# Kernel tuning notes

Hardware: AMD Instinct MI355X
Metric: run time of the kernel (lower is better)

## Reference

```python
import jax, jax.numpy as jnp
import numpy as np

NUM_HEADS = 4
KERNEL = 7


def setup_inputs() -> dict:
    key = jax.random.key(0)
    k = jax.random.split(key, 6)
    B, H, W, C = 4, 64, 64, 128
    kk = KERNEL
    x = jax.random.normal(k[0], (B, H, W, C), dtype=jnp.float32)
    w_qkv = jax.random.normal(k[1], (C, 3 * C), dtype=jnp.float32) * 0.02
    b_qkv = jnp.zeros((3 * C,), dtype=jnp.float32)
    rpb = jax.random.normal(k[2], (NUM_HEADS, 2 * kk - 1, 2 * kk - 1), dtype=jnp.float32) * 0.02
    w_proj = jax.random.normal(k[3], (C, C), dtype=jnp.float32) * 0.02
    b_proj = jnp.zeros((C,), dtype=jnp.float32)
    return {"x": x, "w_qkv": w_qkv, "b_qkv": b_qkv, "rpb": rpb,
            "w_proj": w_proj, "b_proj": b_proj}


def reference(x, w_qkv, b_qkv, rpb, w_proj, b_proj):
    B, H, W, C = x.shape
    nh, k = NUM_HEADS, KERNEL
    d = C // nh
    scale = d ** -0.5

    qkv = x @ w_qkv + b_qkv                      # [B,H,W,3C]
    q, kt, v = jnp.split(qkv, 3, axis=-1)
    q = q.reshape(B, H, W, nh, d) * scale
    kt = kt.reshape(B, H, W, nh, d)
    v = v.reshape(B, H, W, nh, d)

    # NATTEN window: centered, clamped at borders (window never shrinks)
    start_h = jnp.clip(jnp.arange(H) - k // 2, 0, H - k)
    start_w = jnp.clip(jnp.arange(W) - k // 2, 0, W - k)
    idx_h = start_h[:, None] + jnp.arange(k)     # [H,k] key rows per query row
    idx_w = start_w[:, None] + jnp.arange(k)     # [W,k]

    kn = kt[:, idx_h][:, :, :, idx_w]            # [B,H,k,W,k,nh,d]
    vn = v[:, idx_h][:, :, :, idx_w]             # [B,H,k,W,k,nh,d]

    scores = jnp.einsum('bxyhd,bxiyjhd->bxyhij', q, kn)  # [B,H,W,nh,k,k]

    # relative position bias: index = (key_pos - query_pos) + (k-1)
    bh = idx_h - jnp.arange(H)[:, None] + (k - 1)        # [H,k] in [0,2k-2]
    bw = idx_w - jnp.arange(W)[:, None] + (k - 1)        # [W,k]
    bias = rpb[:, bh[:, None, :, None], bw[None, :, None, :]]  # [nh,H,W,k,k]
    scores = scores + jnp.transpose(bias, (1, 2, 0, 3, 4))

    attn = jax.nn.softmax(scores.reshape(B, H, W, nh, k * k), axis=-1)
    attn = attn.reshape(B, H, W, nh, k, k)

    out = jnp.einsum('bxyhij,bxiyjhd->bxyhd', attn, vn)  # [B,H,W,nh,d]
    out = out.reshape(B, H, W, C) @ w_proj + b_proj
    return out
```

## Files before the change

### kernel.cpp

```cpp
#include <hip/hip_runtime.h>
#include <cstddef>
#include <cstdint>

#define Hdim 64
#define Wdim 64
#define NH 4
#define DH 32
#define KW 7
#define QSCALE 0.17677669529663687f

typedef _Float16 v2h __attribute__((ext_vector_type(2)));
typedef _Float16 half8 __attribute__((ext_vector_type(8)));
typedef float f32x4 __attribute__((ext_vector_type(4)));

#if defined(__has_builtin)
#if __has_builtin(__builtin_amdgcn_fdot2)
#define HAVE_FDOT2 1
#endif
#endif

__device__ __forceinline__ float fdot2acc(v2h a, v2h b, float c) {
#ifdef HAVE_FDOT2
    return __builtin_amdgcn_fdot2(a, b, c, false);
#else
    return fmaf((float)a.x, (float)b.x, fmaf((float)a.y, (float)b.y, c));
#endif
}

union F16x8 {
    uint4 u;
    v2h h[4];
};

__global__ __launch_bounds__(256) void prep_weights(
    const float* __restrict__ wq, const float* __restrict__ wp,
    _Float16* __restrict__ wqT, _Float16* __restrict__ wpT)
{
    __shared__ float Ts[64][65];
    int blk = blockIdx.x;
    const float* src;
    _Float16* dst;
    int N, kt, nt;
    if (blk < 12) { src = wq; dst = wqT; N = 384; kt = blk / 6; nt = blk % 6; }
    else { blk -= 12; src = wp; dst = wpT; N = 128; kt = blk >> 1; nt = blk & 1; }
    const int k0 = kt * 64, n0 = nt * 64;
    const int tid = threadIdx.x;

#pragma unroll
    for (int it = 0; it < 16; ++it) {
        int idx = it * 256 + tid;
        int r = idx >> 6, c = idx & 63;
        Ts[r][c] = src[(size_t)(k0 + r) * N + n0 + c];
    }
    __syncthreads();
#pragma unroll
    for (int it = 0; it < 2; ++it) {
        int idx = it * 256 + tid;
        int n = idx >> 3;
        int kq = (idx & 7) * 8;
        _Float16 tmp[8];
#pragma unroll
        for (int j = 0; j < 8; ++j) tmp[j] = (_Float16)Ts[kq + j][n];
        *(uint4*)(dst + (size_t)(n0 + n) * 128 + k0 + kq) = *(const uint4*)tmp;
    }
}

__global__ __launch_bounds__(256) void gemm_qkv_mfma(
    const float* __restrict__ A,
    const _Float16* __restrict__ WT,
    const float* __restrict__ bias,
    _Float16* __restrict__ qkvh)
{
    __shared__ _Float16 As[64 * 136];
    const int m0 = blockIdx.x * 64;
    const int sel = blockIdx.y;
    const int n0 = sel * 128;
    const int tid = threadIdx.x;
    const int wv = tid >> 6;
    const int ln = tid & 15;
    const int quad = (tid & 63) >> 4;

#pragma unroll
    for (int it = 0; it < 8; ++it) {
        int idx = it * 256 + tid;
        int m = idx >> 5;
        int kq = (idx & 31) * 4;
        float4 a = *(const float4*)(A + (size_t)(m0 + m) * 128 + kq);
        _Float16 t[4] = {(_Float16)a.x, (_Float16)a.y, (_Float16)a.z, (_Float16)a.w};
        *(uint2*)(As + m * 136 + kq) = *(const uint2*)t;
    }
    __syncthreads();

    f32x4 acc[8] = {};
    const int mrow = wv * 16 + ln;
#pragma unroll
    for (int ks = 0; ks < 4; ++ks) {
        const half8 af = *(const half8*)(As + mrow * 136 + ks * 32 + quad * 8);
#pragma unroll
        for (int nt = 0; nt < 8; ++nt) {
            const half8 bf = *(const half8*)(WT + (size_t)(n0 + nt * 16 + ln) * 128 + ks * 32 + quad * 8);
            acc[nt] = __builtin_amdgcn_mfma_f32_16x16x32_f16(af, bf, acc[nt], 0, 0, 0);
        }
    }
    __syncthreads();

    const float qscale = (sel == 0) ? QSCALE : 1.0f;
#pragma unroll
    for (int nt = 0; nt < 8; ++nt) {
        const int n = nt * 16 + ln;
        const float bv = bias[n0 + n];
#pragma unroll
        for (int r = 0; r < 4; ++r) {
            const int m = wv * 16 + quad * 4 + r;
            As[m * 136 + n] = (_Float16)((acc[nt][r] + bv) * qscale);
        }
    }
    __syncthreads();

    const int b = m0 >> 12;
    const int yx0 = m0 & 4095;
#pragma unroll
    for (int h = 0; h < 4; ++h) {
        const int r = tid >> 2;
        const int c = tid & 3;
        uint4 v = *(const uint4*)(As + r * 136 + h * 32 + c * 8);
        *(uint4*)(qkvh + (((size_t)sel * 16 + b * 4 + h) * 4096 + yx0 + r) * 32 + c * 8) = v;
    }
}

#define ATS 8
#define AMAXPOS 196
#define KST 40

__global__ __launch_bounds__(256, 4) void local_attn(
    const _Float16* __restrict__ qkvh,
    const float* __restrict__ rpb,
    float* __restrict__ outp)
{
    __shared__ _Float16 kS[AMAXPOS * KST];
    __shared__ _Float16 vS[AMAXPOS * KST];
    __shared__ float rS[169];

    const int bh = blockIdx.x;
    const int h = bh & 3;
    const int ty0 = blockIdx.y * ATS;
    const int tx0 = blockIdx.z * ATS;
    const int tid = threadIdx.x;

    const int lo_h = max(0, min(ty0 - 3, Hdim - KW));
    const int hi_h = min(ty0 + ATS - 4, Hdim - KW) + KW - 1;
    const int lo_w = max(0, min(tx0 - 3, Wdim - KW));
    const int hi_w = min(tx0 + ATS - 4, Wdim - KW) + KW - 1;
    const int ch = hi_h - lo_h + 1;
    const int cw = hi_w - lo_w + 1;
    const int npos = ch * cw;

    const _Float16* kbase = qkvh + (size_t)(16 + bh) * 131072;
    const _Float16* vbase = qkvh + (size_t)(32 + bh) * 131072;

    for (int idx = tid; idx < npos * 4; idx += 256) {
        const int pos = idx >> 2;
        const int c = idx & 3;
        const int ry = pos / cw;
        const int rx = pos - ry * cw;
        const size_t g = ((size_t)(lo_h + ry) * Wdim + (lo_w + rx)) * 32 + c * 8;
        *(uint4*)(kS + pos * KST + c * 8) = *(const uint4*)(kbase + g);
        *(uint4*)(vS + pos * KST + c * 8) = *(const uint4*)(vbase + g);
    }
    for (int i = tid; i < 169; i += 256) rS[i] = rpb[h * 169 + i];
    __syncthreads();

    const int p = tid >> 2;
    const int q = tid & 3;
    const int py = p >> 3, px = p & 7;
    const int y = ty0 + py, x = tx0 + px;
    const int sh = max(0, min(y - 3, Hdim - KW));
    const int sw = max(0, min(x - 3, Wdim - KW));
    const int rb = sh - lo_h;
    const int cb = sw - lo_w;
    const int bh0 = sh - y + 6;
    const int bw0 = sw - x + 6;

    F16x8 qf;
    qf.u = *(const uint4*)(qkvh + (size_t)bh * 131072 + ((size_t)y * Wdim + x) * 32 + q * 8);

    float sc[49];
#pragma unroll
    for (int i = 0; i < KW; ++i) {
        const _Float16* kp = kS + ((rb + i) * cw + cb) * KST + q * 8;
        const int bi = (bh0 + i) * 13 + bw0;
#pragma unroll
        for (int j = 0; j < KW; ++j) {
            F16x8 kf;
            kf.u = *(const uint4*)(kp + j * KST);
            float s = fdot2acc(qf.h[0], kf.h[0],
                      fdot2acc(qf.h[1], kf.h[1],
                      fdot2acc(qf.h[2], kf.h[2],
                      fdot2acc(qf.h[3], kf.h[3], 0.0f))));
            s += __shfl_xor(s, 1);
            s += __shfl_xor(s, 2);
            sc[i * KW + j] = s + rS[bi + j];
        }
    }

    float mx = sc[0];
#pragma unroll
    for (int t = 1; t < 49; ++t) mx = fmaxf(mx, sc[t]);
    float l = 0.f;
#pragma unroll
    for (int t = 0; t < 49; ++t) { sc[t] = __expf(sc[t] - mx); l += sc[t]; }
    const float inv = 1.f / l;

    float o[8] = {};
#pragma unroll
    for (int i = 0; i < KW; ++i) {
        const _Float16* vp = vS + ((rb + i) * cw + cb) * KST + q * 8;
#pragma unroll
        for (int j = 0; j < KW; ++j) {
            F16x8 vf;
            vf.u = *(const uint4*)(vp + j * KST);
            const float w = sc[i * KW + j] * inv;
#pragma unroll
            for (int d = 0; d < 4; ++d) {
                o[2 * d + 0] = fmaf(w, (float)vf.h[d].x, o[2 * d + 0]);
                o[2 * d + 1] = fmaf(w, (float)vf.h[d].y, o[2 * d + 1]);
            }
        }
    }

    const size_t pix = (size_t)(bh >> 2) * 4096 + (size_t)y * Wdim + x;
    float* dst = outp + pix * 128 + h * DH + q * 8;
    *(float4*)(dst)     = make_float4(o[0], o[1], o[2], o[3]);
    *(float4*)(dst + 4) = make_float4(o[4], o[5], o[6], o[7]);
}

__global__ __launch_bounds__(256) void gemm_proj_mfma(
    const float* __restrict__ Af,
    const _Float16* __restrict__ WT,
    const float* __restrict__ bias,
    float* __restrict__ C)
{
    __shared__ float Cs[64 * 132];
    _Float16* As = (_Float16*)Cs;

    const int m0 = blockIdx.x * 64;
    const int tid = threadIdx.x;
    const int wv = tid >> 6;
    const int ln = tid & 15;
    const int quad = (tid & 63) >> 4;

#pragma unroll
    for (int it = 0; it < 8; ++it) {
        int idx = it * 256 + tid;
        int m = idx >> 5;
        int kq = (idx & 31) * 4;
        float4 a = *(const float4*)(Af + (size_t)(m0 + m) * 128 + kq);
        _Float16 t[4] = {(_Float16)a.x, (_Float16)a.y, (_Float16)a.z, (_Float16)a.w};
        *(uint2*)(As + m * 136 + kq) = *(const uint2*)t;
    }
    __syncthreads();

    f32x4 acc[8] = {};
    const int mrow = wv * 16 + ln;
#pragma unroll
    for (int ks = 0; ks < 4; ++ks) {
        const half8 af = *(const half8*)(As + mrow * 136 + ks * 32 + quad * 8);
#pragma unroll
        for (int nt = 0; nt < 8; ++nt) {
            const half8 bf = *(const half8*)(WT + (size_t)(nt * 16 + ln) * 128 + ks * 32 + quad * 8);
            acc[nt] = __builtin_amdgcn_mfma_f32_16x16x32_f16(af, bf, acc[nt], 0, 0, 0);
        }
    }
    __syncthreads();

#pragma unroll
    for (int nt = 0; nt < 8; ++nt) {
        const int n = nt * 16 + ln;
        const float bv = bias[n];
#pragma unroll
        for (int r = 0; r < 4; ++r) {
            const int m = wv * 16 + quad * 4 + r;
            Cs[m * 132 + n] = acc[nt][r] + bv;
        }
    }
    __syncthreads();

#pragma unroll
    for (int it = 0; it < 8; ++it) {
        int idx = it * 256 + tid;
        int m = idx >> 5;
        int c = idx & 31;
        float4 v = *(const float4*)(Cs + m * 132 + c * 4);
        *(float4*)(C + (size_t)(m0 + m) * 128 + c * 4) = v;
    }
}

extern "C" void kernel_launch(void* const* d_in, const int* in_sizes, int n_in,
                              void* d_out, int out_size, void* d_ws, size_t ws_size,
                              hipStream_t stream) {
    const float* x      = (const float*)d_in[0];
    const float* w_qkv  = (const float*)d_in[1];
    const float* b_qkv  = (const float*)d_in[2];
    const float* rpb    = (const float*)d_in[3];
    const float* w_proj = (const float*)d_in[4];
    const float* b_proj = (const float*)d_in[5];
    float* out = (float*)d_out;

    char* ws = (char*)d_ws;
    _Float16* qkvh = (_Float16*)ws;
    float* attnf   = (float*)(ws + 12582912);
    _Float16* wqT  = (_Float16*)(ws + 12582912 + 8388608);
    _Float16* wpT  = (_Float16*)(ws + 12582912 + 8388608 + 98304);

    dim3 blk(256);
    prep_weights<<<16, blk, 0, stream>>>(w_qkv, w_proj, wqT, wpT);
    gemm_qkv_mfma<<<dim3(16384 / 64, 3), blk, 0, stream>>>(x, wqT, b_qkv, qkvh);
    local_attn<<<dim3(16, Hdim / ATS, Wdim / ATS), blk, 0, stream>>>(qkvh, rpb, attnf);
    gemm_proj_mfma<<<dim3(16384 / 64, 1), blk, 0, stream>>>(attnf, wpT, b_proj, out);
}
```

Baseline: 119.7 us.

## Fuse neighborhood attention with output projection in one 1024-thread block

Merges the local attention kernel and the projection GEMM into a single kernel. Each block now handles all four heads for an 8x8 pixel tile, so the attention result stays in shared memory as fp16 and feeds MFMA projection tiles directly. This removes the fp32 intermediate buffer write/read and one kernel launch. In exchange the block uses about 107KB of shared memory and 1024 threads, which limits occupancy to roughly one block per CU, and the grid shrinks to 256 blocks.

```diff
diff --git a/kernel.cpp b/kernel.cpp
--- a/kernel.cpp
+++ b/kernel.cpp
@@ -130,19 +130,23 @@
 
 #define ATS 8
 #define AMAXPOS 196
-#define KST 40
-
-__global__ __launch_bounds__(256, 4) void local_attn(
+#define PSTR 136
+
+__global__ __launch_bounds__(1024) void attn_proj(
     const _Float16* __restrict__ qkvh,
     const float* __restrict__ rpb,
+    const _Float16* __restrict__ wpT,
+    const float* __restrict__ bproj,
     float* __restrict__ outp)
 {
-    __shared__ _Float16 kS[AMAXPOS * KST];
-    __shared__ _Float16 vS[AMAXPOS * KST];
-    __shared__ float rS[169];
-
-    const int bh = blockIdx.x;
-    const int h = bh & 3;
+    __shared__ __align__(16) char arena[AMAXPOS * PSTR * 2 * 2 + 169 * NH * 4];
+    _Float16* kS = (_Float16*)arena;
+    _Float16* vS = kS + AMAXPOS * PSTR;
+    float* rS = (float*)(arena + AMAXPOS * PSTR * 2 * 2);
+    _Float16* Of = kS;
+    float* Cs = (float*)vS;
+
+    const int b = blockIdx.x;
     const int ty0 = blockIdx.y * ATS;
     const int tx0 = blockIdx.z * ATS;
     const int tid = threadIdx.x;
@@ -155,22 +159,24 @@
     const int cw = hi_w - lo_w + 1;
     const int npos = ch * cw;
 
-    const _Float16* kbase = qkvh + (size_t)(16 + bh) * 131072;
-    const _Float16* vbase = qkvh + (size_t)(32 + bh) * 131072;
-
-    for (int idx = tid; idx < npos * 4; idx += 256) {
-        const int pos = idx >> 2;
-        const int c = idx & 3;
+    for (int idx = tid; idx < npos * 16; idx += 1024) {
+        const int pos = idx >> 4;
+        const int sub = idx & 15;
+        const int hh = sub >> 2;
+        const int cc = sub & 3;
         const int ry = pos / cw;
         const int rx = pos - ry * cw;
-        const size_t g = ((size_t)(lo_h + ry) * Wdim + (lo_w + rx)) * 32 + c * 8;
-        *(uint4*)(kS + pos * KST + c * 8) = *(const uint4*)(kbase + g);
-        *(uint4*)(vS + pos * KST + c * 8) = *(const uint4*)(vbase + g);
-    }
-    for (int i = tid; i < 169; i += 256) rS[i] = rpb[h * 169 + i];
-    __syncthreads();
-
-    const int p = tid >> 2;
+        const size_t g = ((size_t)(lo_h + ry) * Wdim + (lo_w + rx)) * 32 + cc * 8;
+        const size_t kpl = ((size_t)(16 + b * 4 + hh)) * 131072;
+        const size_t vpl = ((size_t)(32 + b * 4 + hh)) * 131072;
+        *(uint4*)(kS + pos * PSTR + hh * 32 + cc * 8) = *(const uint4*)(qkvh + kpl + g);
+        *(uint4*)(vS + pos * PSTR + hh * 32 + cc * 8) = *(const uint4*)(qkvh + vpl + g);
+    }
+    for (int i = tid; i < 169 * NH; i += 1024) rS[i] = rpb[i];
+    __syncthreads();
+
+    const int h = tid >> 8;
+    const int p = (tid >> 2) & 63;
     const int q = tid & 3;
     const int py = p >> 3, px = p & 7;
     const int y = ty0 + py, x = tx0 + px;
@@ -180,19 +186,21 @@
     const int cb = sw - lo_w;
     const int bh0 = sh - y + 6;
     const int bw0 = sw - x + 6;
+    const int hq = h * 32 + q * 8;
 
     F16x8 qf;
-    qf.u = *(const uint4*)(qkvh + (size_t)bh * 131072 + ((size_t)y * Wdim + x) * 32 + q * 8);
+    qf.u = *(const uint4*)(qkvh + ((size_t)(b * 4 + h)) * 131072 +
+                           ((size_t)y * Wdim + x) * 32 + q * 8);
 
     float sc[49];
 #pragma unroll
     for (int i = 0; i < KW; ++i) {
-        const _Float16* kp = kS + ((rb + i) * cw + cb) * KST + q * 8;
-        const int bi = (bh0 + i) * 13 + bw0;
+        const _Float16* kp = kS + ((rb + i) * cw + cb) * PSTR + hq;
+        const int bi = h * 169 + (bh0 + i) * 13 + bw0;
 #pragma unroll
         for (int j = 0; j < KW; ++j) {
             F16x8 kf;
-            kf.u = *(const uint4*)(kp + j * KST);
+            kf.u = *(const uint4*)(kp + j * PSTR);
             float s = fdot2acc(qf.h[0], kf.h[0],
                       fdot2acc(qf.h[1], kf.h[1],
                       fdot2acc(qf.h[2], kf.h[2],
@@ -214,11 +222,11 @@
     float o[8] = {};
 #pragma unroll
     for (int i = 0; i < KW; ++i) {
-        const _Float16* vp = vS + ((rb + i) * cw + cb) * KST + q * 8;
+        const _Float16* vp = vS + ((rb + i) * cw + cb) * PSTR + hq;
 #pragma unroll
         for (int j = 0; j < KW; ++j) {
             F16x8 vf;
-            vf.u = *(const uint4*)(vp + j * KST);
+            vf.u = *(const uint4*)(vp + j * PSTR);
             const float w = sc[i * KW + j] * inv;
 #pragma unroll
             for (int d = 0; d < 4; ++d) {
@@ -228,70 +236,55 @@
         }
     }
 
-    const size_t pix = (size_t)(bh >> 2) * 4096 + (size_t)y * Wdim + x;
-    float* dst = outp + pix * 128 + h * DH + q * 8;
-    *(float4*)(dst)     = make_float4(o[0], o[1], o[2], o[3]);
-    *(float4*)(dst + 4) = make_float4(o[4], o[5], o[6], o[7]);
-}
-
-__global__ __launch_bounds__(256) void gemm_proj_mfma(
-    const float* __restrict__ Af,
-    const _Float16* __restrict__ WT,
-    const float* __restrict__ bias,
-    float* __restrict__ C)
-{
-    __shared__ float Cs[64 * 132];
-    _Float16* As = (_Float16*)Cs;
-
-    const int m0 = blockIdx.x * 64;
-    const int tid = threadIdx.x;
-    const int wv = tid >> 6;
+    __syncthreads();
+    {
+        _Float16 oh[8];
+#pragma unroll
+        for (int d = 0; d < 8; ++d) oh[d] = (_Float16)o[d];
+        *(uint4*)(Of + p * PSTR + hq) = *(const uint4*)oh;
+    }
+    __syncthreads();
+
+    const int wvid = tid >> 6;
+    const int mt = wvid >> 2;
+    const int nh2 = wvid & 3;
     const int ln = tid & 15;
     const int quad = (tid & 63) >> 4;
 
-#pragma unroll
-    for (int it = 0; it < 8; ++it) {
-        int idx = it * 256 + tid;
-        int m = idx >> 5;
-        int kq = (idx & 31) * 4;
-        float4 a = *(const float4*)(Af + (size_t)(m0 + m) * 128 + kq);
-        _Float16 t[4] = {(_Float16)a.x, (_Float16)a.y, (_Float16)a.z, (_Float16)a.w};
-        *(uint2*)(As + m * 136 + kq) = *(const uint2*)t;
-    }
-    __syncthreads();
-
-    f32x4 acc[8] = {};
-    const int mrow = wv * 16 + ln;
-#pragma unroll
-    for (int ks = 0; ks < 4; ++ks) {
-        const half8 af = *(const half8*)(As + mrow * 136 + ks * 32 + quad * 8);
-#pragma unroll
-        for (int nt = 0; nt < 8; ++nt) {
-            const half8 bf = *(const half8*)(WT + (size_t)(nt * 16 + ln) * 128 + ks * 32 + quad * 8);
-            acc[nt] = __builtin_amdgcn_mfma_f32_16x16x32_f16(af, bf, acc[nt], 0, 0, 0);
-        }
-    }
-    __syncthreads();
-
-#pragma unroll
-    for (int nt = 0; nt < 8; ++nt) {
-        const int n = nt * 16 + ln;
-        const float bv = bias[n];
-#pragma unroll
-        for (int r = 0; r < 4; ++r) {
-            const int m = wv * 16 + quad * 4 + r;
-            Cs[m * 132 + n] = acc[nt][r] + bv;
-        }
-    }
-    __syncthreads();
-
-#pragma unroll
-    for (int it = 0; it < 8; ++it) {
-        int idx = it * 256 + tid;
+    half8 afr[4];
+#pragma unroll
+    for (int ks = 0; ks < 4; ++ks)
+        afr[ks] = *(const half8*)(Of + (mt * 16 + ln) * PSTR + ks * 32 + quad * 8);
+
+    f32x4 acc[2] = {};
+#pragma unroll
+    for (int nt = 0; nt < 2; ++nt) {
+        const int n = nh2 * 32 + nt * 16 + ln;
+#pragma unroll
+        for (int ks = 0; ks < 4; ++ks) {
+            const half8 bf = *(const half8*)(wpT + (size_t)n * 128 + ks * 32 + quad * 8);
+            acc[nt] = __builtin_amdgcn_mfma_f32_16x16x32_f16(afr[ks], bf, acc[nt], 0, 0, 0);
+        }
+    }
+
+#pragma unroll
+    for (int nt = 0; nt < 2; ++nt) {
+        const int n = nh2 * 32 + nt * 16 + ln;
+        const float bv = bproj[n];
+#pragma unroll
+        for (int r = 0; r < 4; ++r)
+            Cs[(mt * 16 + quad * 4 + r) * 132 + n] = acc[nt][r] + bv;
+    }
+    __syncthreads();
+
+#pragma unroll
+    for (int it = 0; it < 2; ++it) {
+        int idx = it * 1024 + tid;
         int m = idx >> 5;
         int c = idx & 31;
         float4 v = *(const float4*)(Cs + m * 132 + c * 4);
-        *(float4*)(C + (size_t)(m0 + m) * 128 + c * 4) = v;
+        const size_t pix = (size_t)b * 4096 + (size_t)(ty0 + (m >> 3)) * Wdim + tx0 + (m & 7);
+        *(float4*)(outp + pix * 128 + c * 4) = v;
     }
 }
 
@@ -308,13 +301,11 @@
 
     char* ws = (char*)d_ws;
     _Float16* qkvh = (_Float16*)ws;
-    float* attnf   = (float*)(ws + 12582912);
-    _Float16* wqT  = (_Float16*)(ws + 12582912 + 8388608);
-    _Float16* wpT  = (_Float16*)(ws + 12582912 + 8388608 + 98304);
-
-    dim3 blk(256);
-    prep_weights<<<16, blk, 0, stream>>>(w_qkv, w_proj, wqT, wpT);
-    gemm_qkv_mfma<<<dim3(16384 / 64, 3), blk, 0, stream>>>(x, wqT, b_qkv, qkvh);
-    local_attn<<<dim3(16, Hdim / ATS, Wdim / ATS), blk, 0, stream>>>(qkvh, rpb, attnf);
-    gemm_proj_mfma<<<dim3(16384 / 64, 1), blk, 0, stream>>>(attnf, wpT, b_proj, out);
-}
+    _Float16* wqT  = (_Float16*)(ws + 12582912);
+    _Float16* wpT  = (_Float16*)(ws + 12582912 + 98304);
+
+    prep_weights<<<16, dim3(256), 0, stream>>>(w_qkv, w_proj, wqT, wpT);
+    gemm_qkv_mfma<<<dim3(16384 / 64, 3), dim3(256), 0, stream>>>(x, wqT, b_qkv, qkvh);
+    attn_proj<<<dim3(4, Hdim / ATS, Wdim / ATS), dim3(1024), 0, stream>>>(
+        qkvh, rpb, wpT, b_proj, out);
+}
```

New measurement: 240.1 us. 101% more time.
